# Optimization experiments

Measured on AMD Instinct MI355X. Metric: run time of the kernel, lower is better.

## Reference

```python
import jax, jax.numpy as jnp
import numpy as np

N_HEAD = 16
WINDOW = 256
GLOBAL = 32


def _sparse_mask(T):
    # local window of +/- WINDOW//2 plus global rows/cols for first GLOBAL tokens
    i = jnp.arange(T)
    local = jnp.abs(i[:, None] - i[None, :]) <= (WINDOW // 2)
    glob = (i[:, None] < GLOBAL) | (i[None, :] < GLOBAL)
    return local | glob  # [T, T] bool


def setup_inputs() -> dict:
    key = jax.random.key(0)
    k1, k2, k3 = jax.random.split(key, 3)
    B, T, C = 1, 4096, 1024
    scale = 0.02
    return {
        "x": jax.random.normal(k1, (B, T, C), dtype=jnp.float32),
        "W_attn": jax.random.normal(k2, (C, 3 * C), dtype=jnp.float32) * scale,
        "b_attn": jnp.zeros((3 * C,), dtype=jnp.float32),
        "W_proj": jax.random.normal(k3, (C, C), dtype=jnp.float32) * scale,
        "b_proj": jnp.zeros((C,), dtype=jnp.float32),
    }


def reference(x, W_attn, b_attn, W_proj, b_proj):
    B, T, C = x.shape
    H = N_HEAD
    D = C // H

    qkv = x @ W_attn + b_attn  # [B, T, 3C]
    q, k, v = jnp.split(qkv, 3, axis=-1)
    # [B, H, T, D]
    q = q.reshape(B, T, H, D).transpose(0, 2, 1, 3)
    k = k.reshape(B, T, H, D).transpose(0, 2, 1, 3)
    v = v.reshape(B, T, H, D).transpose(0, 2, 1, 3)

    mask = _sparse_mask(T)  # [T, T]
    att = jnp.einsum("bhqd,bhkd->bhqk", q, k) * (1.0 / np.sqrt(D))
    neg = jnp.finfo(att.dtype).min
    att = jnp.where(mask, att, neg)
    att = jax.nn.softmax(att, axis=-1)
    y = jnp.einsum("bhqk,bhkd->bhqd", att, v)  # [B, H, T, D]
    y = y.transpose(0, 2, 1, 3).reshape(B, T, C)
    return y @ W_proj + b_proj
```

## Files before the change

kernel.cpp:

```cpp
#include <hip/hip_runtime.h>
#include <hip/hip_bf16.h>
#include <math.h>

#define T_SEQ 4096
#define C_DIM 1024
#define H_HEADS 16
#define D_HEAD 64
#define QKVW 3072
#define WIN_HALF 128
#define GLOBAL_TOK 32

typedef __attribute__((ext_vector_type(8))) short bf16x8;
typedef __attribute__((ext_vector_type(4))) float f32x4;

__device__ __forceinline__ float bf2f(unsigned short u) {
    union { unsigned int i; float f; } c; c.i = ((unsigned int)u) << 16; return c.f;
}
__device__ __forceinline__ unsigned short f2bf(float f) {
    union { float f; unsigned int i; } c; c.f = f;
    return (unsigned short)((c.i + 0x7fffu + ((c.i >> 16) & 1u)) >> 16);
}

__device__ __forceinline__ void gll16(const unsigned short* g, unsigned short* l) {
    __builtin_amdgcn_global_load_lds(
        (const __attribute__((address_space(1))) void*)g,
        (__attribute__((address_space(3))) void*)l, 16, 0, 0);
}

__device__ __forceinline__ int swz(int row, int chunk) {
    return row * 64 + ((chunk ^ (row & 7)) * 8);
}

__global__ __launch_bounds__(256) void prep_kernel(
    const float* __restrict__ x, const float* __restrict__ Wa,
    const float* __restrict__ Wp,
    unsigned short* __restrict__ xb, unsigned short* __restrict__ Wabt,
    unsigned short* __restrict__ Wpbt)
{
    __shared__ unsigned short tile[32][36];
    const int bid = blockIdx.x;
    const int t = threadIdx.x;
    if (bid < 4096) {
        const int idx = bid * 256 + t;
        float4 v = ((const float4*)x)[idx];
        ushort4 o;
        o.x = f2bf(v.x); o.y = f2bf(v.y); o.z = f2bf(v.z); o.w = f2bf(v.w);
        ((ushort4*)xb)[idx] = o;
        return;
    }
    const float* src; unsigned short* dst; int R, Ncols, bx, by;
    if (bid < 4096 + 3072) {
        const int b = bid - 4096;
        src = Wa; dst = Wabt; R = C_DIM; Ncols = QKVW;
        bx = b % (QKVW / 32); by = b / (QKVW / 32);
    } else {
        const int b = bid - 7168;
        src = Wp; dst = Wpbt; R = C_DIM; Ncols = C_DIM;
        bx = b % (C_DIM / 32); by = b / (C_DIM / 32);
    }
    const int r0 = by * 32, c0 = bx * 32;
    const int rr = t >> 3, cq = (t & 7) * 4;
    float4 v = *(const float4*)(src + (size_t)(r0 + rr) * Ncols + c0 + cq);
    tile[rr][cq + 0] = f2bf(v.x); tile[rr][cq + 1] = f2bf(v.y);
    tile[rr][cq + 2] = f2bf(v.z); tile[rr][cq + 3] = f2bf(v.w);
    __syncthreads();
    const int cc = t >> 3, rq = (t & 7) * 4;
    ushort4 o;
    o.x = tile[rq + 0][cc]; o.y = tile[rq + 1][cc];
    o.z = tile[rq + 2][cc]; o.w = tile[rq + 3][cc];
    *(ushort4*)(dst + (size_t)(c0 + cc) * R + r0 + rq) = o;
}

#define GBK 64
#define GSTAGE(BUF, KO)                                                        \
  _Pragma("unroll")                                                            \
  for (int i = 0; i < 4; ++i) {                                                \
    const int r = w * 32 + i * 8 + sr;                                         \
    gll16(Ab + (size_t)r * K + (KO) + sc8, &As[BUF][(w * 32 + i * 8) * GBK]);  \
    gll16(Bb + (size_t)r * K + (KO) + sc8, &Bs[BUF][(w * 32 + i * 8) * GBK]);  \
  }

template<int OUT_BF16, int WRITE_VT>
__device__ __forceinline__ void gemm_body(
    const unsigned short* __restrict__ A,
    const unsigned short* __restrict__ Bt,
    const float* __restrict__ bias,
    void* __restrict__ Cv, unsigned short* __restrict__ vTp,
    int M, int N, int K)
{
    __shared__ unsigned short As[2][128 * GBK];
    __shared__ unsigned short Bs[2][128 * GBK];
    const int tid = threadIdx.x;
    const int w = tid >> 6, lane = tid & 63;
    const int quad = lane >> 4, r16 = lane & 15;
    const int m0 = blockIdx.y * 128, n0 = blockIdx.x * 128;
    const int wm = (w & 1) * 64, wn = (w >> 1) * 64;
    const int sr = lane >> 3;
    const int sc8 = ((lane & 7) ^ sr) * 8;

    f32x4 acc[4][4];
    #pragma unroll
    for (int i = 0; i < 4; ++i)
        #pragma unroll
        for (int j = 0; j < 4; ++j) acc[i][j] = (f32x4){0.f, 0.f, 0.f, 0.f};

    const unsigned short* Ab = A + (size_t)m0 * K;
    const unsigned short* Bb = Bt + (size_t)n0 * K;

    const int NS = K / GBK;
    GSTAGE(0, 0);
    GSTAGE(1, GBK);

    for (int t = 0; t < NS; ++t) {
        if (t == NS - 1) { asm volatile("s_waitcnt vmcnt(0)" ::: "memory"); }
        else             { asm volatile("s_waitcnt vmcnt(8)" ::: "memory"); }
        __builtin_amdgcn_sched_barrier(0);
        __syncthreads();
        const int cb = t & 1;
        #pragma unroll
        for (int kk = 0; kk < 2; ++kk) {
            bf16x8 af[4], bf_[4];
            #pragma unroll
            for (int tt = 0; tt < 4; ++tt) {
                const int ra = wm + tt * 16 + r16;
                af[tt]  = *(const bf16x8*)&As[cb][ra * GBK + (((kk * 4 + quad) ^ (ra & 7)) * 8)];
                const int rb = wn + tt * 16 + r16;
                bf_[tt] = *(const bf16x8*)&Bs[cb][rb * GBK + (((kk * 4 + quad) ^ (rb & 7)) * 8)];
            }
            #pragma unroll
            for (int mt = 0; mt < 4; ++mt)
                #pragma unroll
                for (int nt = 0; nt < 4; ++nt)
                    acc[mt][nt] = __builtin_amdgcn_mfma_f32_16x16x32_bf16(
                        af[mt], bf_[nt], acc[mt][nt], 0, 0, 0);
        }
        if (t + 2 < NS) {
            __syncthreads();
            GSTAGE(cb, (t + 2) * GBK);
        }
    }

    if (WRITE_VT && n0 >= 2 * C_DIM) {
        #pragma unroll
        for (int nt = 0; nt < 4; ++nt) {
            const int col = n0 + wn + nt * 16 + r16;
            const float bv = bias[col];
            const int vcol = col - 2 * C_DIM;
            #pragma unroll
            for (int mt = 0; mt < 4; ++mt) {
                ushort4 o;
                o.x = f2bf(acc[mt][nt][0] + bv);
                o.y = f2bf(acc[mt][nt][1] + bv);
                o.z = f2bf(acc[mt][nt][2] + bv);
                o.w = f2bf(acc[mt][nt][3] + bv);
                *(ushort4*)&vTp[(size_t)vcol * T_SEQ + m0 + wm + mt * 16 + quad * 4] = o;
            }
        }
    } else {
        #pragma unroll
        for (int nt = 0; nt < 4; ++nt) {
            const int col = n0 + wn + nt * 16 + r16;
            const float bv = bias[col];
            #pragma unroll
            for (int mt = 0; mt < 4; ++mt)
                #pragma unroll
                for (int reg = 0; reg < 4; ++reg) {
                    const int row = m0 + wm + mt * 16 + quad * 4 + reg;
                    if (OUT_BF16)
                        ((unsigned short*)Cv)[(size_t)row * N + col] = f2bf(acc[mt][nt][reg] + bv);
                    else
                        ((float*)Cv)[(size_t)row * N + col] = acc[mt][nt][reg] + bv;
                }
        }
    }
}

__global__ __launch_bounds__(256) void gemm_qkv_kernel(
    const unsigned short* __restrict__ A, const unsigned short* __restrict__ Bt,
    const float* __restrict__ bias, void* __restrict__ Cv,
    unsigned short* __restrict__ vTp, int M, int N, int K)
{
    gemm_body<1, 1>(A, Bt, bias, Cv, vTp, M, N, K);
}
__global__ __launch_bounds__(256) void gemm_proj_kernel(
    const unsigned short* __restrict__ A, const unsigned short* __restrict__ Bt,
    const float* __restrict__ bias, void* __restrict__ Cv,
    unsigned short* __restrict__ vTp, int M, int N, int K)
{
    gemm_body<0, 0>(A, Bt, bias, Cv, vTp, M, N, K);
}

#define PT_STRIDE 72
#define NSLOT 8
#define PROW 72

struct KVbuf { bf16x8 kl[4], kh[4], vl[4], vh[4]; };
struct StReg { bf16x8 a, b, c, d; };

#define LOAD_KV(C0, B)                                                         \
  {                                                                            \
    const unsigned short* kr_ = kb + (size_t)((C0) + n) * QKVW + quad * 8;     \
    _Pragma("unroll")                                                          \
    for (int g = 0; g < 4; ++g) {                                              \
      B.kl[g] = *(const bf16x8*)(kr_ + (size_t)(g * 16) * QKVW);               \
      B.kh[g] = *(const bf16x8*)(kr_ + (size_t)(g * 16) * QKVW + 32);          \
    }                                                                          \
    const unsigned short* vr_ = vb + (size_t)n * T_SEQ + (C0) + quad * 8;      \
    _Pragma("unroll")                                                          \
    for (int d = 0; d < 4; ++d) {                                              \
      B.vl[d] = *(const bf16x8*)(vr_ + (size_t)(d * 16) * T_SEQ);              \
      B.vh[d] = *(const bf16x8*)(vr_ + (size_t)(d * 16) * T_SEQ + 32);         \
    }                                                                          \
  }

#define SOFTMAX_P_UPDATE(StV)                                                  \
    if (!__all(mm <= m_run + 8.f)) {                                           \
      float mx_ = fmaxf(mm, __shfl_xor(mm, 16));                               \
      mx_ = fmaxf(mx_, __shfl_xor(mx_, 32));                                   \
      const float mn_ = fmaxf(m_run, mx_);                                     \
      const float al_ = __expf(m_run - mn_);                                   \
      l_part *= al_;                                                           \
      _Pragma("unroll")                                                        \
      for (int d = 0; d < 4; ++d)                                              \
        _Pragma("unroll")                                                      \
        for (int r = 0; r < 4; ++r) O[d][r] *= al_;                            \
      m_run = mn_;                                                             \
    }                                                                          \
    {                                                                          \
      const float mnf = m_run;                                                 \
      float rs = 0.f;                                                          \
      _Pragma("unroll")                                                        \
      for (int g = 0; g < 4; ++g) {                                            \
        const float e0 = __expf(StV[g][0] - mnf);                              \
        const float e1 = __expf(StV[g][1] - mnf);                              \
        const float e2 = __expf(StV[g][2] - mnf);                              \
        const float e3 = __expf(StV[g][3] - mnf);                              \
        rs += (e0 + e1) + (e2 + e3);                                           \
        const unsigned int p01 = f2bf(e0) | ((unsigned int)f2bf(e1) << 16);    \
        const unsigned int p23 = f2bf(e2) | ((unsigned int)f2bf(e3) << 16);    \
        *(unsigned int*)&myPt[n * PT_STRIDE + g * 16 + quad * 4] = p01;        \
        *(unsigned int*)&myPt[n * PT_STRIDE + g * 16 + quad * 4 + 2] = p23;    \
      }                                                                        \
      l_part += rs;                                                            \
    }

#define PROC_TILE(ITV, CUR, NXT)                                               \
  {                                                                            \
    const int it_ = (ITV);                                                     \
    const int c0 = split * 512 + it_ * 64;                                     \
    f32x4 St[4];                                                               \
    __builtin_amdgcn_s_setprio(1);                                             \
    _Pragma("unroll")                                                          \
    for (int g = 0; g < 4; ++g) {                                              \
      St[g] = __builtin_amdgcn_mfma_f32_16x16x32_bf16(CUR.kl[g], q0, Zf, 0, 0, 0); \
      St[g] = __builtin_amdgcn_mfma_f32_16x16x32_bf16(CUR.kh[g], q1, St[g], 0, 0, 0); \
    }                                                                          \
    __builtin_amdgcn_s_setprio(0);                                             \
    if (it_ + 1 < n_tiles) {                                                   \
      LOAD_KV(c0 + 64, NXT);                                                   \
    }                                                                          \
    float mm = -INFINITY;                                                      \
    _Pragma("unroll")                                                          \
    for (int g = 0; g < 4; ++g)                                                \
      _Pragma("unroll")                                                        \
      for (int r = 0; r < 4; ++r) {                                            \
        const float v = St[g][r] * 0.125f;                                     \
        St[g][r] = v; mm = fmaxf(mm, v);                                       \
      }                                                                        \
    SOFTMAX_P_UPDATE(St)                                                       \
    asm volatile("s_waitcnt lgkmcnt(0)" ::: "memory");                         \
    __builtin_amdgcn_sched_barrier(0);                                         \
    __builtin_amdgcn_s_setprio(1);                                             \
    _Pragma("unroll")                                                          \
    for (int kg = 0; kg < 2; ++kg) {                                           \
      bf16x8 pf_ = *(const bf16x8*)&myPt[n * PT_STRIDE + kg * 32 + quad * 8];  \
      _Pragma("unroll")                                                        \
      for (int d = 0; d < 4; ++d)                                              \
        O[d] = __builtin_amdgcn_mfma_f32_16x16x32_bf16(                        \
            kg ? CUR.vh[d] : CUR.vl[d], pf_, O[d], 0, 0, 0);                   \
    }                                                                          \
    __builtin_amdgcn_s_setprio(0);                                             \
  }

#define STAGE_LOAD(C0, R)                                                      \
  { const int c0s_ = (C0);                                                     \
    R.a = *(const bf16x8*)(kb + (size_t)(c0s_ + srow) * QKVW + scol * 8);      \
    R.b = *(const bf16x8*)(kb + (size_t)(c0s_ + srow + 32) * QKVW + scol * 8); \
    R.c = *(const bf16x8*)(vb + (size_t)srow * T_SEQ + c0s_ + scol * 8);       \
    R.d = *(const bf16x8*)(vb + (size_t)(srow + 32) * T_SEQ + c0s_ + scol * 8); }

#define STAGE_WRITE(BUF, R)                                                    \
  { *(bf16x8*)&Ks[BUF][kdst0] = R.a;                                           \
    *(bf16x8*)&Ks[BUF][kdst1] = R.b;                                           \
    *(bf16x8*)&Vs[BUF][kdst0] = R.c;                                           \
    *(bf16x8*)&Vs[BUF][kdst1] = R.d; }

#define WTILE(ITV, BUF, RW, RL)                                                \
  {                                                                            \
    const int it_ = (ITV);                                                     \
    const int c0 = (it_ == 0) ? 0 : (blo + (it_ - 1) * 64);                    \
    if (activeW) {                                                             \
      bf16x8 kl[4], kh[4];                                                     \
      _Pragma("unroll")                                                        \
      for (int g = 0; g < 4; ++g) {                                            \
        kl[g] = *(const bf16x8*)&Ks[BUF][swz(n + g * 16, quad)];               \
        kh[g] = *(const bf16x8*)&Ks[BUF][swz(n + g * 16, quad + 4)];           \
      }                                                                        \
      f32x4 St[4];                                                             \
      __builtin_amdgcn_s_setprio(1);                                           \
      _Pragma("unroll")                                                        \
      for (int g = 0; g < 4; ++g) {                                            \
        St[g] = __builtin_amdgcn_mfma_f32_16x16x32_bf16(kl[g], q0, Zf, 0, 0, 0); \
        St[g] = __builtin_amdgcn_mfma_f32_16x16x32_bf16(kh[g], q1, St[g], 0, 0, 0); \
      }                                                                        \
      __builtin_amdgcn_s_setprio(0);                                           \
      float mm = -INFINITY;                                                    \
      if (it_ != 0 && c0 >= rowbase - 113 && c0 <= rowbase + 65) {             \
        _Pragma("unroll")                                                      \
        for (int g = 0; g < 4; ++g)                                            \
          _Pragma("unroll")                                                    \
          for (int r = 0; r < 4; ++r) {                                        \
            const float v = St[g][r] * 0.125f;                                 \
            St[g][r] = v; mm = fmaxf(mm, v);                                   \
          }                                                                    \
      } else if (it_ == 0 && rowbase >= 192) {                                 \
        _Pragma("unroll")                                                      \
        for (int g = 0; g < 2; ++g)                                            \
          _Pragma("unroll")                                                    \
          for (int r = 0; r < 4; ++r) {                                        \
            const float v = St[g][r] * 0.125f;                                 \
            St[g][r] = v; mm = fmaxf(mm, v);                                   \
          }                                                                    \
        _Pragma("unroll")                                                      \
        for (int g = 2; g < 4; ++g)                                            \
          _Pragma("unroll")                                                    \
          for (int r = 0; r < 4; ++r) St[g][r] = -INFINITY;                    \
      } else {                                                                 \
        _Pragma("unroll")                                                      \
        for (int g = 0; g < 4; ++g)                                            \
          _Pragma("unroll")                                                    \
          for (int r = 0; r < 4; ++r) {                                        \
            float v = St[g][r] * 0.125f;                                       \
            const int col = c0 + g * 16 + quad * 4 + r;                        \
            int dd = row - col; dd = dd < 0 ? -dd : dd;                        \
            if (!(col < GLOBAL_TOK || dd <= WIN_HALF)) v = -INFINITY;          \
            St[g][r] = v; mm = fmaxf(mm, v);                                   \
          }                                                                    \
      }                                                                        \
      SOFTMAX_P_UPDATE(St)                                                     \
      bf16x8 vl[4], vh[4];                                                     \
      _Pragma("unroll")                                                        \
      for (int d = 0; d < 4; ++d) {                                            \
        vl[d] = *(const bf16x8*)&Vs[BUF][swz(n + d * 16, quad)];               \
        vh[d] = *(const bf16x8*)&Vs[BUF][swz(n + d * 16, quad + 4)];           \
      }                                                                        \
      asm volatile("s_waitcnt lgkmcnt(0)" ::: "memory");                       \
      __builtin_amdgcn_sched_barrier(0);                                       \
      __builtin_amdgcn_s_setprio(1);                                           \
      _Pragma("unroll")                                                        \
      for (int kg = 0; kg < 2; ++kg) {                                         \
        bf16x8 pf_ = *(const bf16x8*)&myPt[n * PT_STRIDE + kg * 32 + quad * 8];\
        _Pragma("unroll")                                                      \
        for (int d = 0; d < 4; ++d)                                            \
          O[d] = __builtin_amdgcn_mfma_f32_16x16x32_bf16(                      \
              kg ? vh[d] : vl[d], pf_, O[d], 0, 0, 0);                         \
      }                                                                        \
      __builtin_amdgcn_s_setprio(0);                                           \
    }                                                                          \
    if (it_ + 1 < NT) {                                                        \
      asm volatile("s_waitcnt vmcnt(0)" ::: "memory");                         \
      __builtin_amdgcn_sched_barrier(0);                                       \
      STAGE_WRITE((BUF) ^ 1, RW);                                              \
      if (it_ + 2 < NT) { STAGE_LOAD(blo + (it_ + 1) * 64, RL); }              \
      __syncthreads();                                                         \
    }                                                                          \
  }

__global__ __launch_bounds__(256, 3) void sparse_attn_mfma(
    const unsigned short* __restrict__ qkv,
    const unsigned short* __restrict__ vT,
    unsigned short* __restrict__ y,
    float* __restrict__ part)
{
    __shared__ unsigned short Ks[2][64 * 64];
    __shared__ unsigned short Vs[2][64 * 64];
    __shared__ unsigned short Pt[4][16 * PT_STRIDE];
    const int tid = threadIdx.x;
    const int w = tid >> 6, lane = tid & 63;
    const int quad = lane >> 4, n = lane & 15;
    const int bid = blockIdx.x;
    const f32x4 Zf = (f32x4){0.f, 0.f, 0.f, 0.f};

    if (bid >= 64) {
        const int wb = bid - 64;
        const int h = wb & 15;
        const int B = wb >> 4;
        const int base = B * 64;
        const int rowbase = base + w * 16;
        const bool activeW = !(B == 0 && w < 2);
        int blo = base - 128; if (blo < 64) blo = 64;
        int bhi = base + 192; if (bhi > T_SEQ) bhi = T_SEQ;
        const int NT = 1 + (bhi - blo) / 64;

        const unsigned short* kb = qkv + C_DIM + h * 64;
        const unsigned short* vb = vT + (size_t)h * 64 * T_SEQ;
        unsigned short* myPt = Pt[w];

        const int srow = tid >> 3, scol = tid & 7;
        const int kdst0 = swz(srow, scol);
        const int kdst1 = kdst0 + 32 * 64;

        const unsigned short* qp = qkv + (size_t)(rowbase + n) * QKVW + h * 64 + quad * 8;
        bf16x8 q0 = *(const bf16x8*)qp;
        bf16x8 q1 = *(const bf16x8*)(qp + 32);

        f32x4 O[4];
        #pragma unroll
        for (int i = 0; i < 4; ++i) O[i] = (f32x4){0.f, 0.f, 0.f, 0.f};
        float m_run = -INFINITY, l_part = 0.f;
        const int row = rowbase + n;

        StReg r0, r1;
        STAGE_LOAD(0, r0);
        asm volatile("s_waitcnt vmcnt(0)" ::: "memory");
        __builtin_amdgcn_sched_barrier(0);
        STAGE_WRITE(0, r0);
        STAGE_LOAD(blo, r1);
        __syncthreads();

        int it = 0;
        for (;;) {
            WTILE(it, 0, r1, r0);
            if (++it >= NT) break;
            WTILE(it, 1, r0, r1);
            if (++it >= NT) break;
        }

        if (activeW) {
            float l_run = l_part;
            l_run += __shfl_xor(l_run, 16);
            l_run += __shfl_xor(l_run, 32);
            const float invL = 1.f / l_run;
            #pragma unroll
            for (int dblk = 0; dblk < 4; ++dblk)
                #pragma unroll
                for (int r = 0; r < 4; ++r)
                    y[(size_t)row * C_DIM + h * 64 + dblk * 16 + quad * 4 + r] =
                        f2bf(O[dblk][r] * invL);
        }
    } else {
        const int idx = bid;
        const int h = idx & 15;
        const int u = (idx >> 4) * 4 + w;
        const int rt = u >> 3, split = u & 7;
        const int rowbase = rt * 16;
        const int n_tiles = 8;

        const unsigned short* qp = qkv + (size_t)(rowbase + n) * QKVW + h * 64 + quad * 8;
        bf16x8 q0 = *(const bf16x8*)qp;
        bf16x8 q1 = *(const bf16x8*)(qp + 32);

        const unsigned short* kb = qkv + C_DIM + h * 64;
        const unsigned short* vb = vT + (size_t)h * 64 * T_SEQ;
        unsigned short* myPt = Pt[w];

        f32x4 O[4];
        #pragma unroll
        for (int i = 0; i < 4; ++i) O[i] = (f32x4){0.f, 0.f, 0.f, 0.f};
        float m_run = -INFINITY, l_part = 0.f;

        KVbuf b0, b1;
        LOAD_KV(split * 512, b0);
        int it = 0;
        for (;;) {
            PROC_TILE(it, b0, b1);
            if (++it >= n_tiles) break;
            PROC_TILE(it, b1, b0);
            if (++it >= n_tiles) break;
        }

        float l_run = l_part;
        l_run += __shfl_xor(l_run, 16);
        l_run += __shfl_xor(l_run, 32);

        float* pb = part + ((size_t)(h * 2 + rt) * NSLOT + split) * 16 * PROW;
        #pragma unroll
        for (int dblk = 0; dblk < 4; ++dblk)
            #pragma unroll
            for (int r = 0; r < 4; ++r)
                pb[n * PROW + dblk * 16 + quad * 4 + r] = O[dblk][r];
        if (quad == 0) {
            pb[n * PROW + 64] = m_run;
            pb[n * PROW + 65] = l_run;
        }
    }
}

__global__ __launch_bounds__(64) void attn_combine(
    const float* __restrict__ part, unsigned short* __restrict__ y)
{
    const int d = threadIdx.x;
    const int h = blockIdx.x >> 1, rt = blockIdx.x & 1;
    const float* base = part + (size_t)(h * 2 + rt) * NSLOT * 16 * PROW;
    for (int row = 0; row < 16; ++row) {
        float M = -INFINITY;
        for (int sl = 0; sl < NSLOT; ++sl)
            M = fmaxf(M, base[(size_t)sl * 16 * PROW + row * PROW + 64]);
        float L = 0.f, Od = 0.f;
        for (int sl = 0; sl < NSLOT; ++sl) {
            const float* p = base + (size_t)sl * 16 * PROW + row * PROW;
            const float s = __expf(p[64] - M);
            L += p[65] * s;
            Od += p[d] * s;
        }
        y[(size_t)(rt * 16 + row) * C_DIM + h * 64 + d] = f2bf(Od / L);
    }
}

extern "C" void kernel_launch(void* const* d_in, const int* in_sizes, int n_in,
                              void* d_out, int out_size, void* d_ws, size_t ws_size,
                              hipStream_t stream) {
    const float* x  = (const float*)d_in[0];
    const float* Wa = (const float*)d_in[1];
    const float* ba = (const float*)d_in[2];
    const float* Wp = (const float*)d_in[3];
    const float* bp = (const float*)d_in[4];
    float* out = (float*)d_out;

    unsigned short* xb   = (unsigned short*)d_ws;
    unsigned short* Wabt = xb   + (size_t)T_SEQ * C_DIM;
    unsigned short* Wpbt = Wabt + (size_t)C_DIM * QKVW;
    unsigned short* qkv  = Wpbt + (size_t)C_DIM * C_DIM;
    unsigned short* yat  = qkv  + (size_t)T_SEQ * QKVW;
    unsigned short* vT   = yat  + (size_t)T_SEQ * C_DIM;
    float* part = (float*)(vT + (size_t)C_DIM * T_SEQ);

    prep_kernel<<<4096 + 3072 + 1024, 256, 0, stream>>>(
        x, Wa, Wp, xb, Wabt, Wpbt);

    gemm_qkv_kernel<<<dim3(QKVW / 128, T_SEQ / 128), 256, 0, stream>>>(
        xb, Wabt, ba, qkv, vT, T_SEQ, QKVW, C_DIM);

    const int nBlocks = 1024 + 64;
    sparse_attn_mfma<<<nBlocks, 256, 0, stream>>>(qkv, vT, yat, part);
    attn_combine<<<H_HEADS * 2, 64, 0, stream>>>(part, yat);

    gemm_proj_kernel<<<dim3(C_DIM / 128, T_SEQ / 128), 256, 0, stream>>>(
        yat, Wpbt, bp, out, nullptr, T_SEQ, C_DIM, C_DIM);
}
```

Baseline: 186.1 us.

## Process two query row groups per wave in windowed attention blocks

Each windowed-attention block now covers 128 query rows instead of 64, and each wave handles two 16-row groups (A and B) that share the same K/V tiles loaded from LDS. This halves the number of window blocks and reuses each staged K/V tile across twice as many queries. The cost is a wider K/V range per block (more tiles, some partly masked), roughly double the accumulator registers per wave, and fewer blocks available to fill the GPU.

```diff
diff --git a/kernel.cpp b/kernel.cpp
--- a/kernel.cpp
+++ b/kernel.cpp
@@ -213,21 +213,21 @@
     }                                                                          \
   }
 
-#define SOFTMAX_P_UPDATE(StV)                                                  \
-    if (!__all(mm <= m_run + 8.f)) {                                           \
+#define SOFTMAX_P_UPDATE(StV, OV, MR, LP)                                      \
+    if (!__all(mm <= (MR) + 8.f)) {                                            \
       float mx_ = fmaxf(mm, __shfl_xor(mm, 16));                               \
       mx_ = fmaxf(mx_, __shfl_xor(mx_, 32));                                   \
-      const float mn_ = fmaxf(m_run, mx_);                                     \
-      const float al_ = __expf(m_run - mn_);                                   \
-      l_part *= al_;                                                           \
+      const float mn_ = fmaxf((MR), mx_);                                      \
+      const float al_ = __expf((MR) - mn_);                                    \
+      (LP) *= al_;                                                             \
       _Pragma("unroll")                                                        \
       for (int d = 0; d < 4; ++d)                                              \
         _Pragma("unroll")                                                      \
-        for (int r = 0; r < 4; ++r) O[d][r] *= al_;                            \
-      m_run = mn_;                                                             \
+        for (int r = 0; r < 4; ++r) (OV)[d][r] *= al_;                         \
+      (MR) = mn_;                                                              \
     }                                                                          \
     {                                                                          \
-      const float mnf = m_run;                                                 \
+      const float mnf = (MR);                                                  \
       float rs = 0.f;                                                          \
       _Pragma("unroll")                                                        \
       for (int g = 0; g < 4; ++g) {                                            \
@@ -241,8 +241,60 @@
         *(unsigned int*)&myPt[n * PT_STRIDE + g * 16 + quad * 4] = p01;        \
         *(unsigned int*)&myPt[n * PT_STRIDE + g * 16 + quad * 4 + 2] = p23;    \
       }                                                                        \
-      l_part += rs;                                                            \
-    }
+      (LP) += rs;                                                              \
+    }
+
+#define MASKSM(StV, OV, MR, LP, RGB, ROWV)                                     \
+    {                                                                          \
+      float mm = -INFINITY;                                                    \
+      if (it_ != 0 && c0 >= (RGB) - 113 && c0 <= (RGB) + 65) {                 \
+        _Pragma("unroll")                                                      \
+        for (int g = 0; g < 4; ++g)                                            \
+          _Pragma("unroll")                                                    \
+          for (int r = 0; r < 4; ++r) {                                        \
+            const float v = StV[g][r] * 0.125f;                                \
+            StV[g][r] = v; mm = fmaxf(mm, v);                                  \
+          }                                                                    \
+      } else if (it_ == 0 && (RGB) >= 192) {                                   \
+        _Pragma("unroll")                                                      \
+        for (int g = 0; g < 2; ++g)                                            \
+          _Pragma("unroll")                                                    \
+          for (int r = 0; r < 4; ++r) {                                        \
+            const float v = StV[g][r] * 0.125f;                                \
+            StV[g][r] = v; mm = fmaxf(mm, v);                                  \
+          }                                                                    \
+        _Pragma("unroll")                                                      \
+        for (int g = 2; g < 4; ++g)                                            \
+          _Pragma("unroll")                                                    \
+          for (int r = 0; r < 4; ++r) StV[g][r] = -INFINITY;                   \
+      } else {                                                                 \
+        _Pragma("unroll")                                                      \
+        for (int g = 0; g < 4; ++g)                                            \
+          _Pragma("unroll")                                                    \
+          for (int r = 0; r < 4; ++r) {                                        \
+            float v = StV[g][r] * 0.125f;                                      \
+            const int col = c0 + g * 16 + quad * 4 + r;                        \
+            int dd = (ROWV) - col; dd = dd < 0 ? -dd : dd;                     \
+            if (!(col < GLOBAL_TOK || dd <= WIN_HALF)) v = -INFINITY;          \
+            StV[g][r] = v; mm = fmaxf(mm, v);                                  \
+          }                                                                    \
+      }                                                                        \
+      SOFTMAX_P_UPDATE(StV, OV, MR, LP)                                        \
+    }
+
+#define PVACC(OV, VB)                                                          \
+    asm volatile("s_waitcnt lgkmcnt(0)" ::: "memory");                         \
+    __builtin_amdgcn_sched_barrier(0);                                         \
+    __builtin_amdgcn_s_setprio(1);                                             \
+    _Pragma("unroll")                                                          \
+    for (int kg = 0; kg < 2; ++kg) {                                           \
+      bf16x8 pf_ = *(const bf16x8*)&myPt[n * PT_STRIDE + kg * 32 + quad * 8];  \
+      _Pragma("unroll")                                                        \
+      for (int d = 0; d < 4; ++d)                                              \
+        (OV)[d] = __builtin_amdgcn_mfma_f32_16x16x32_bf16(                     \
+            kg ? VB.vh[d] : VB.vl[d], pf_, (OV)[d], 0, 0, 0);                  \
+    }                                                                          \
+    __builtin_amdgcn_s_setprio(0);
 
 #define PROC_TILE(ITV, CUR, NXT)                                               \
   {                                                                            \
@@ -267,7 +319,7 @@
         const float v = St[g][r] * 0.125f;                                     \
         St[g][r] = v; mm = fmaxf(mm, v);                                       \
       }                                                                        \
-    SOFTMAX_P_UPDATE(St)                                                       \
+    SOFTMAX_P_UPDATE(St, O, m_run, l_part)                                     \
     asm volatile("s_waitcnt lgkmcnt(0)" ::: "memory");                         \
     __builtin_amdgcn_sched_barrier(0);                                         \
     __builtin_amdgcn_s_setprio(1);                                             \
@@ -299,73 +351,38 @@
   {                                                                            \
     const int it_ = (ITV);                                                     \
     const int c0 = (it_ == 0) ? 0 : (blo + (it_ - 1) * 64);                    \
-    if (activeW) {                                                             \
-      bf16x8 kl[4], kh[4];                                                     \
+    {                                                                          \
+      KVbuf lb_;                                                               \
       _Pragma("unroll")                                                        \
       for (int g = 0; g < 4; ++g) {                                            \
-        kl[g] = *(const bf16x8*)&Ks[BUF][swz(n + g * 16, quad)];               \
-        kh[g] = *(const bf16x8*)&Ks[BUF][swz(n + g * 16, quad + 4)];           \
-      }                                                                        \
-      f32x4 St[4];                                                             \
+        lb_.kl[g] = *(const bf16x8*)&Ks[BUF][swz(n + g * 16, quad)];           \
+        lb_.kh[g] = *(const bf16x8*)&Ks[BUF][swz(n + g * 16, quad + 4)];       \
+      }                                                                        \
+      f32x4 StA[4];                                                            \
       __builtin_amdgcn_s_setprio(1);                                           \
       _Pragma("unroll")                                                        \
       for (int g = 0; g < 4; ++g) {                                            \
-        St[g] = __builtin_amdgcn_mfma_f32_16x16x32_bf16(kl[g], q0, Zf, 0, 0, 0); \
-        St[g] = __builtin_amdgcn_mfma_f32_16x16x32_bf16(kh[g], q1, St[g], 0, 0, 0); \
+        StA[g] = __builtin_amdgcn_mfma_f32_16x16x32_bf16(lb_.kl[g], qA0, Zf, 0, 0, 0); \
+        StA[g] = __builtin_amdgcn_mfma_f32_16x16x32_bf16(lb_.kh[g], qA1, StA[g], 0, 0, 0); \
       }                                                                        \
       __builtin_amdgcn_s_setprio(0);                                           \
-      float mm = -INFINITY;                                                    \
-      if (it_ != 0 && c0 >= rowbase - 113 && c0 <= rowbase + 65) {             \
-        _Pragma("unroll")                                                      \
-        for (int g = 0; g < 4; ++g)                                            \
-          _Pragma("unroll")                                                    \
-          for (int r = 0; r < 4; ++r) {                                        \
-            const float v = St[g][r] * 0.125f;                                 \
-            St[g][r] = v; mm = fmaxf(mm, v);                                   \
-          }                                                                    \
-      } else if (it_ == 0 && rowbase >= 192) {                                 \
-        _Pragma("unroll")                                                      \
-        for (int g = 0; g < 2; ++g)                                            \
-          _Pragma("unroll")                                                    \
-          for (int r = 0; r < 4; ++r) {                                        \
-            const float v = St[g][r] * 0.125f;                                 \
-            St[g][r] = v; mm = fmaxf(mm, v);                                   \
-          }                                                                    \
-        _Pragma("unroll")                                                      \
-        for (int g = 2; g < 4; ++g)                                            \
-          _Pragma("unroll")                                                    \
-          for (int r = 0; r < 4; ++r) St[g][r] = -INFINITY;                    \
-      } else {                                                                 \
-        _Pragma("unroll")                                                      \
-        for (int g = 0; g < 4; ++g)                                            \
-          _Pragma("unroll")                                                    \
-          for (int r = 0; r < 4; ++r) {                                        \
-            float v = St[g][r] * 0.125f;                                       \
-            const int col = c0 + g * 16 + quad * 4 + r;                        \
-            int dd = row - col; dd = dd < 0 ? -dd : dd;                        \
-            if (!(col < GLOBAL_TOK || dd <= WIN_HALF)) v = -INFINITY;          \
-            St[g][r] = v; mm = fmaxf(mm, v);                                   \
-          }                                                                    \
-      }                                                                        \
-      SOFTMAX_P_UPDATE(St)                                                     \
-      bf16x8 vl[4], vh[4];                                                     \
+      if (actA) { MASKSM(StA, OA, m_runA, l_partA, rgbA, rowA) }               \
+      f32x4 StB[4];                                                            \
+      __builtin_amdgcn_s_setprio(1);                                           \
+      _Pragma("unroll")                                                        \
+      for (int g = 0; g < 4; ++g) {                                            \
+        StB[g] = __builtin_amdgcn_mfma_f32_16x16x32_bf16(lb_.kl[g], qB0, Zf, 0, 0, 0); \
+        StB[g] = __builtin_amdgcn_mfma_f32_16x16x32_bf16(lb_.kh[g], qB1, StB[g], 0, 0, 0); \
+      }                                                                        \
+      __builtin_amdgcn_s_setprio(0);                                           \
       _Pragma("unroll")                                                        \
       for (int d = 0; d < 4; ++d) {                                            \
-        vl[d] = *(const bf16x8*)&Vs[BUF][swz(n + d * 16, quad)];               \
-        vh[d] = *(const bf16x8*)&Vs[BUF][swz(n + d * 16, quad + 4)];           \
-      }                                                                        \
-      asm volatile("s_waitcnt lgkmcnt(0)" ::: "memory");                       \
-      __builtin_amdgcn_sched_barrier(0);                                       \
-      __builtin_amdgcn_s_setprio(1);                                           \
-      _Pragma("unroll")                                                        \
-      for (int kg = 0; kg < 2; ++kg) {                                         \
-        bf16x8 pf_ = *(const bf16x8*)&myPt[n * PT_STRIDE + kg * 32 + quad * 8];\
-        _Pragma("unroll")                                                      \
-        for (int d = 0; d < 4; ++d)                                            \
-          O[d] = __builtin_amdgcn_mfma_f32_16x16x32_bf16(                      \
-              kg ? vh[d] : vl[d], pf_, O[d], 0, 0, 0);                         \
-      }                                                                        \
-      __builtin_amdgcn_s_setprio(0);                                           \
+        lb_.vl[d] = *(const bf16x8*)&Vs[BUF][swz(n + d * 16, quad)];           \
+        lb_.vh[d] = *(const bf16x8*)&Vs[BUF][swz(n + d * 16, quad + 4)];       \
+      }                                                                        \
+      if (actA) { PVACC(OA, lb_) }                                             \
+      MASKSM(StB, OB, m_runB, l_partB, rgbB, rowB)                             \
+      PVACC(OB, lb_)                                                           \
     }                                                                          \
     if (it_ + 1 < NT) {                                                        \
       asm volatile("s_waitcnt vmcnt(0)" ::: "memory");                         \
@@ -395,11 +412,12 @@
         const int wb = bid - 64;
         const int h = wb & 15;
         const int B = wb >> 4;
-        const int base = B * 64;
-        const int rowbase = base + w * 16;
-        const bool activeW = !(B == 0 && w < 2);
+        const int base = B * 128;
+        const int rgbA = base + w * 16;
+        const int rgbB = rgbA + 64;
+        const bool actA = !(B == 0 && w < 2);
         int blo = base - 128; if (blo < 64) blo = 64;
-        int bhi = base + 192; if (bhi > T_SEQ) bhi = T_SEQ;
+        int bhi = base + 256; if (bhi > T_SEQ) bhi = T_SEQ;
         const int NT = 1 + (bhi - blo) / 64;
 
         const unsigned short* kb = qkv + C_DIM + h * 64;
@@ -410,15 +428,22 @@
         const int kdst0 = swz(srow, scol);
         const int kdst1 = kdst0 + 32 * 64;
 
-        const unsigned short* qp = qkv + (size_t)(rowbase + n) * QKVW + h * 64 + quad * 8;
-        bf16x8 q0 = *(const bf16x8*)qp;
-        bf16x8 q1 = *(const bf16x8*)(qp + 32);
-
-        f32x4 O[4];
-        #pragma unroll
-        for (int i = 0; i < 4; ++i) O[i] = (f32x4){0.f, 0.f, 0.f, 0.f};
-        float m_run = -INFINITY, l_part = 0.f;
-        const int row = rowbase + n;
+        const int rowA = rgbA + n, rowB = rgbB + n;
+        const unsigned short* qpA = qkv + (size_t)rowA * QKVW + h * 64 + quad * 8;
+        bf16x8 qA0 = *(const bf16x8*)qpA;
+        bf16x8 qA1 = *(const bf16x8*)(qpA + 32);
+        const unsigned short* qpB = qkv + (size_t)rowB * QKVW + h * 64 + quad * 8;
+        bf16x8 qB0 = *(const bf16x8*)qpB;
+        bf16x8 qB1 = *(const bf16x8*)(qpB + 32);
+
+        f32x4 OA[4], OB[4];
+        #pragma unroll
+        for (int i = 0; i < 4; ++i) {
+            OA[i] = (f32x4){0.f, 0.f, 0.f, 0.f};
+            OB[i] = (f32x4){0.f, 0.f, 0.f, 0.f};
+        }
+        float m_runA = -INFINITY, l_partA = 0.f;
+        float m_runB = -INFINITY, l_partB = 0.f;
 
         StReg r0, r1;
         STAGE_LOAD(0, r0);
@@ -436,8 +461,8 @@
             if (++it >= NT) break;
         }
 
-        if (activeW) {
-            float l_run = l_part;
+        if (actA) {
+            float l_run = l_partA;
             l_run += __shfl_xor(l_run, 16);
             l_run += __shfl_xor(l_run, 32);
             const float invL = 1.f / l_run;
@@ -445,8 +470,20 @@
             for (int dblk = 0; dblk < 4; ++dblk)
                 #pragma unroll
                 for (int r = 0; r < 4; ++r)
-                    y[(size_t)row * C_DIM + h * 64 + dblk * 16 + quad * 4 + r] =
-                        f2bf(O[dblk][r] * invL);
+                    y[(size_t)rowA * C_DIM + h * 64 + dblk * 16 + quad * 4 + r] =
+                        f2bf(OA[dblk][r] * invL);
+        }
+        {
+            float l_run = l_partB;
+            l_run += __shfl_xor(l_run, 16);
+            l_run += __shfl_xor(l_run, 32);
+            const float invL = 1.f / l_run;
+            #pragma unroll
+            for (int dblk = 0; dblk < 4; ++dblk)
+                #pragma unroll
+                for (int r = 0; r < 4; ++r)
+                    y[(size_t)rowB * C_DIM + h * 64 + dblk * 16 + quad * 4 + r] =
+                        f2bf(OB[dblk][r] * invL);
         }
     } else {
         const int idx = bid;
@@ -541,7 +578,7 @@
     gemm_qkv_kernel<<<dim3(QKVW / 128, T_SEQ / 128), 256, 0, stream>>>(
         xb, Wabt, ba, qkv, vT, T_SEQ, QKVW, C_DIM);
 
-    const int nBlocks = 1024 + 64;
+    const int nBlocks = 64 + 512;
     sparse_attn_mfma<<<nBlocks, 256, 0, stream>>>(qkv, vT, yat, part);
     attn_combine<<<H_HEADS * 2, 64, 0, stream>>>(part, yat);
 
```

Result: slower. 198.4 us (+6.6%).

## Single-buffer K/V shared tiles and raise occupancy target to five blocks

Applied to the files above, without the earlier changes.

Replaces the double-buffered K and V shared-memory tiles with single buffers and adds a barrier before each staging write so the next tile is written only after all waves finish reading the current one. The register-prefetch of the following tile is kept. Halving the LDS footprint, together with launch bounds raised from 3 to 5 blocks per CU, is meant to allow more resident blocks so latency is hidden by occupancy. The cost is an extra block-wide barrier per tile that serializes compute and LDS writes, and tighter register limits that may cause spilling.

```diff
diff --git a/kernel.cpp b/kernel.cpp
--- a/kernel.cpp
+++ b/kernel.cpp
@@ -289,13 +289,13 @@
     R.c = *(const bf16x8*)(vb + (size_t)srow * T_SEQ + c0s_ + scol * 8);       \
     R.d = *(const bf16x8*)(vb + (size_t)(srow + 32) * T_SEQ + c0s_ + scol * 8); }
 
-#define STAGE_WRITE(BUF, R)                                                    \
-  { *(bf16x8*)&Ks[BUF][kdst0] = R.a;                                           \
-    *(bf16x8*)&Ks[BUF][kdst1] = R.b;                                           \
-    *(bf16x8*)&Vs[BUF][kdst0] = R.c;                                           \
-    *(bf16x8*)&Vs[BUF][kdst1] = R.d; }
-
-#define WTILE(ITV, BUF, RW, RL)                                                \
+#define STAGE_WRITE(R)                                                         \
+  { *(bf16x8*)&Ks[kdst0] = R.a;                                                \
+    *(bf16x8*)&Ks[kdst1] = R.b;                                                \
+    *(bf16x8*)&Vs[kdst0] = R.c;                                                \
+    *(bf16x8*)&Vs[kdst1] = R.d; }
+
+#define WTILE(ITV, RW, RL)                                                     \
   {                                                                            \
     const int it_ = (ITV);                                                     \
     const int c0 = (it_ == 0) ? 0 : (blo + (it_ - 1) * 64);                    \
@@ -303,8 +303,8 @@
       bf16x8 kl[4], kh[4];                                                     \
       _Pragma("unroll")                                                        \
       for (int g = 0; g < 4; ++g) {                                            \
-        kl[g] = *(const bf16x8*)&Ks[BUF][swz(n + g * 16, quad)];               \
-        kh[g] = *(const bf16x8*)&Ks[BUF][swz(n + g * 16, quad + 4)];           \
+        kl[g] = *(const bf16x8*)&Ks[swz(n + g * 16, quad)];                    \
+        kh[g] = *(const bf16x8*)&Ks[swz(n + g * 16, quad + 4)];                \
       }                                                                        \
       f32x4 St[4];                                                             \
       __builtin_amdgcn_s_setprio(1);                                           \
@@ -351,8 +351,8 @@
       bf16x8 vl[4], vh[4];                                                     \
       _Pragma("unroll")                                                        \
       for (int d = 0; d < 4; ++d) {                                            \
-        vl[d] = *(const bf16x8*)&Vs[BUF][swz(n + d * 16, quad)];               \
-        vh[d] = *(const bf16x8*)&Vs[BUF][swz(n + d * 16, quad + 4)];           \
+        vl[d] = *(const bf16x8*)&Vs[swz(n + d * 16, quad)];                    \
+        vh[d] = *(const bf16x8*)&Vs[swz(n + d * 16, quad + 4)];                \
       }                                                                        \
       asm volatile("s_waitcnt lgkmcnt(0)" ::: "memory");                       \
       __builtin_amdgcn_sched_barrier(0);                                       \
@@ -368,22 +368,23 @@
       __builtin_amdgcn_s_setprio(0);                                           \
     }                                                                          \
     if (it_ + 1 < NT) {                                                        \
+      __syncthreads();                       \
       asm volatile("s_waitcnt vmcnt(0)" ::: "memory");                         \
       __builtin_amdgcn_sched_barrier(0);                                       \
-      STAGE_WRITE((BUF) ^ 1, RW);                                              \
+      STAGE_WRITE(RW);                                                         \
       if (it_ + 2 < NT) { STAGE_LOAD(blo + (it_ + 1) * 64, RL); }              \
-      __syncthreads();                                                         \
+      __syncthreads();                                     \
     }                                                                          \
   }
 
-__global__ __launch_bounds__(256, 3) void sparse_attn_mfma(
+__global__ __launch_bounds__(256, 5) void sparse_attn_mfma(
     const unsigned short* __restrict__ qkv,
     const unsigned short* __restrict__ vT,
     unsigned short* __restrict__ y,
     float* __restrict__ part)
 {
-    __shared__ unsigned short Ks[2][64 * 64];
-    __shared__ unsigned short Vs[2][64 * 64];
+    __shared__ unsigned short Ks[64 * 64];
+    __shared__ unsigned short Vs[64 * 64];
     __shared__ unsigned short Pt[4][16 * PT_STRIDE];
     const int tid = threadIdx.x;
     const int w = tid >> 6, lane = tid & 63;
@@ -424,15 +425,15 @@
         STAGE_LOAD(0, r0);
         asm volatile("s_waitcnt vmcnt(0)" ::: "memory");
         __builtin_amdgcn_sched_barrier(0);
-        STAGE_WRITE(0, r0);
+        STAGE_WRITE(r0);
         STAGE_LOAD(blo, r1);
         __syncthreads();
 
         int it = 0;
         for (;;) {
-            WTILE(it, 0, r1, r0);
+            WTILE(it, r1, r0);
             if (++it >= NT) break;
-            WTILE(it, 1, r0, r1);
+            WTILE(it, r0, r1);
             if (++it >= NT) break;
         }
 
```

Result: slower. 239.0 us (+28.4%).
